# Performance work log

Hardware: AMD Instinct MI355X
Metric: run time of the kernel (lower is better)

The kernel has to match this reference:

```python
import jax, jax.numpy as jnp
import numpy as np

EPS = 1e-5
GROUPS = 8

def _bn(x, g, b, axes):
    # training-mode batch norm over `axes`, channel axis = 1
    m = jnp.mean(x, axis=axes, keepdims=True)
    v = jnp.var(x, axis=axes, keepdims=True)
    shp = (1, -1) + (1,) * (x.ndim - 2)
    return (x - m) / jnp.sqrt(v + EPS) * g.reshape(shp) + b.reshape(shp)

def setup_inputs() -> dict:
    key = jax.random.key(0)
    k0, k1, k2 = jax.random.split(key, 3)
    N, C, T, V = 64, 256, 64, 25
    out_planes = 256
    gp = out_planes // GROUPS  # 32
    x = jax.random.normal(k0, (N, C, T, V), jnp.float32)
    w_qkv = jax.random.normal(k1, (2 * out_planes, C), jnp.float32) * np.float32(np.sqrt(1.0 / C))
    relative = jax.random.normal(k2, (2 * gp, 2 * V - 1), jnp.float32) * np.float32(np.sqrt(1.0 / gp))
    return {
        "x": x,
        "w_qkv": w_qkv,
        "relative": relative,
        "bn_qkv_g": jnp.ones(2 * out_planes, jnp.float32),
        "bn_qkv_b": jnp.zeros(2 * out_planes, jnp.float32),
        "bn_sim_g": jnp.ones(3 * GROUPS, jnp.float32),
        "bn_sim_b": jnp.zeros(3 * GROUPS, jnp.float32),
        "bn_out_g": jnp.ones(2 * out_planes, jnp.float32),
        "bn_out_b": jnp.zeros(2 * out_planes, jnp.float32),
    }

def reference(x, w_qkv, relative, bn_qkv_g, bn_qkv_b, bn_sim_g, bn_sim_b, bn_out_g, bn_out_b):
    N, C, T, V = x.shape
    out_planes = w_qkv.shape[0] // 2
    gp = out_planes // GROUPS
    K = V  # kernel_size == V by construction
    # static relative index table
    qi = np.arange(K)[None, :]
    ki = np.arange(K)[:, None]
    flat_idx = (ki - qi + K - 1).reshape(-1)
    # mean over frames T (permute(0,2,1,3) then mean over dim1 == mean over axis 2)
    y = jnp.mean(x, axis=2)  # [N, C, V]
    # 1x1 conv qkv + BN1d
    qkv = _bn(jnp.einsum('oc,ncv->nov', w_qkv, y), bn_qkv_g, bn_qkv_b, (0, 2))
    qkv = qkv.reshape(N, GROUPS, 2 * gp, V)
    q, k, v = qkv[:, :, : gp // 2], qkv[:, :, gp // 2: gp], qkv[:, :, gp:]
    all_emb = relative[:, flat_idx].reshape(2 * gp, K, K)
    q_e, k_e, v_e = all_emb[: gp // 2], all_emb[gp // 2: gp], all_emb[gp:]
    qr = jnp.einsum('ngci,cij->ngij', q, q_e)
    kr = jnp.einsum('ngci,cij->ngij', k, k_e).swapaxes(2, 3)
    qk = jnp.einsum('ngci,ngcj->ngij', q, k)
    stacked = jnp.concatenate([qk, qr, kr], axis=1)  # [N, 3*groups, V, V]
    stacked = _bn(stacked, bn_sim_g, bn_sim_b, (0, 2, 3)).reshape(N, 3, GROUPS, V, V).sum(axis=1)
    sim = jax.nn.softmax(stacked, axis=3)  # [N, groups, V, V]
    sv = jnp.einsum('ngij,ngcj->ngci', sim, v)
    sve = jnp.einsum('ngij,cij->ngci', sim, v_e)
    so = jnp.concatenate([sv, sve], axis=-1).reshape(N, 2 * out_planes, V)
    o = _bn(so, bn_out_g, bn_out_b, (0, 2)).reshape(N, out_planes, 2, V).sum(axis=2)
    o = jax.nn.sigmoid(o)[:, :, None, :]  # [N, out_planes, 1, V]
    return x + x * o
```

## Files before the change

kernel.cpp:

```cpp
#include <hip/hip_runtime.h>
#include <cmath>

#define NN 64
#define CC 256
#define TT 64
#define VV 25
#define OO 512
#define GG 8
#define NV (NN*VV)
#define STK 625

typedef float f4 __attribute__((ext_vector_type(4)));

__global__ __launch_bounds__(256) void k_mean(const float* __restrict__ x,
                                              float* __restrict__ y,
                                              float* __restrict__ accz) {
    __shared__ float tile[TT * VV];
    __shared__ float part[8][VV];
    int b = blockIdx.x;
    if (b == 0) {
        for (int i = threadIdx.x; i < 2096; i += 256) accz[i] = 0.f;
    }
    const float4* x4 = (const float4*)(x + (size_t)b * (TT * VV));
    float4* t4 = (float4*)tile;
    for (int i = threadIdx.x; i < (TT * VV) / 4; i += 256) t4[i] = x4[i];
    __syncthreads();
    int t = threadIdx.x;
    if (t < 200) {
        int v = t % VV, ch = t / VV;
        float s = 0.f;
        #pragma unroll
        for (int k = 0; k < 8; ++k) s += tile[(ch * 8 + k) * VV + v];
        part[ch][v] = s;
    }
    __syncthreads();
    if (t < VV) {
        float s = 0.f;
        #pragma unroll
        for (int k = 0; k < 8; ++k) s += part[k][t];
        y[(size_t)b * VV + t] = s * (1.0f / TT);
    }
}

__global__ __launch_bounds__(256) void k_qkv(const float* __restrict__ y,
                                             const float* __restrict__ w,
                                             float* __restrict__ qkv,
                                             float* __restrict__ qacc) {
    __shared__ float ys[CC][VV + 1];
    __shared__ float qs[64][VV + 1];
    int n = blockIdx.x >> 3, oc = blockIdx.x & 7;
    const float* yp = y + (size_t)n * CC * VV;
    for (int i = threadIdx.x; i < CC * VV; i += 256) ys[i / VV][i % VV] = yp[i];
    __syncthreads();
    int t = threadIdx.x;
    if (t < 200) {
        int v = t % VV, o0 = t / VV;
        const float* wp = w + (size_t)(oc * 64 + o0) * CC;
        float acc[8] = {0, 0, 0, 0, 0, 0, 0, 0};
        for (int c = 0; c < CC; c += 8) {
            float y0 = ys[c][v],     y1 = ys[c + 1][v], y2 = ys[c + 2][v], y3 = ys[c + 3][v];
            float y4_ = ys[c + 4][v], y5 = ys[c + 5][v], y6 = ys[c + 6][v], y7 = ys[c + 7][v];
            #pragma unroll
            for (int u = 0; u < 8; ++u) {
                const float4 wa = *(const float4*)(wp + (size_t)u * 8 * CC + c);
                const float4 wb = *(const float4*)(wp + (size_t)u * 8 * CC + c + 4);
                acc[u] += y0 * wa.x + y1 * wa.y + y2 * wa.z + y3 * wa.w
                        + y4_ * wb.x + y5 * wb.y + y6 * wb.z + y7 * wb.w;
            }
        }
        #pragma unroll
        for (int u = 0; u < 8; ++u) qs[o0 + u * 8][v] = acc[u];
    }
    __syncthreads();
    float* qp = qkv + ((size_t)n * OO + oc * 64) * VV;
    for (int i = t; i < 64 * VV; i += 256) qp[i] = qs[i / VV][i % VV];
    if (t < 64) {
        float s = 0.f, s2 = 0.f;
        #pragma unroll
        for (int v = 0; v < VV; ++v) { float val = qs[t][v]; s += val; s2 += val * val; }
        atomicAdd(&qacc[oc * 64 + t], s);
        atomicAdd(&qacc[512 + oc * 64 + t], s2);
    }
}

__global__ __launch_bounds__(256) void k_scores(const float* __restrict__ qkv,
                                                const float* __restrict__ rel,
                                                const float* __restrict__ qacc,
                                                const float* __restrict__ gq,
                                                const float* __restrict__ bq,
                                                float* __restrict__ stk,
                                                float* __restrict__ sacc) {
    int n = blockIdx.x >> 3, gb = blockIdx.x & 7;
    __shared__ float qs[32][VV + 1];
    __shared__ float rs[32 * 49];
    __shared__ float csc[32], csh[32];
    __shared__ float sred[24];
    int t = threadIdx.x;
    if (t < 32) {
        int ch = gb * 64 + t;
        float m = qacc[ch] * (1.0f / NV);
        float var = qacc[512 + ch] * (1.0f / NV) - m * m;
        float sc = gq[ch] * rsqrtf(var + 1e-5f);
        csc[t] = sc; csh[t] = bq[ch] - m * sc;
    }
    __syncthreads();
    for (int i = t; i < 32 * VV; i += 256) {
        int c = i / VV, v = i - c * VV;
        qs[c][v] = qkv[((size_t)n * OO + gb * 64 + c) * VV + v] * csc[c] + csh[c];
    }
    for (int i = t; i < 32 * 49; i += 256) rs[i] = rel[i];
    __syncthreads();
    float ls0 = 0.f, ls1 = 0.f, ls2 = 0.f, ls3 = 0.f, ls4 = 0.f, ls5 = 0.f;
    size_t base = (size_t)n * 24;
    for (int ij = t; ij < STK; ij += 256) {
        int i = ij / VV, j = ij - (ij / VV) * VV;
        float aqk = 0.f, aqr = 0.f, akr = 0.f;
        #pragma unroll
        for (int c = 0; c < 16; ++c) {
            float qv = qs[c][i], kv = qs[16 + c][j];
            aqk += qv * kv;
            aqr += qv * rs[c * 49 + i - j + 24];
            akr += kv * rs[(16 + c) * 49 + j - i + 24];
        }
        stk[(base + gb) * STK + ij]      = aqk;
        stk[(base + 8 + gb) * STK + ij]  = aqr;
        stk[(base + 16 + gb) * STK + ij] = akr;
        ls0 += aqk; ls1 += aqk * aqk;
        ls2 += aqr; ls3 += aqr * aqr;
        ls4 += akr; ls5 += akr * akr;
    }
    #pragma unroll
    for (int off = 32; off > 0; off >>= 1) {
        ls0 += __shfl_down(ls0, off); ls1 += __shfl_down(ls1, off);
        ls2 += __shfl_down(ls2, off); ls3 += __shfl_down(ls3, off);
        ls4 += __shfl_down(ls4, off); ls5 += __shfl_down(ls5, off);
    }
    int lane = t & 63, wid = t >> 6;
    if (lane == 0) {
        sred[wid * 6 + 0] = ls0; sred[wid * 6 + 1] = ls1;
        sred[wid * 6 + 2] = ls2; sred[wid * 6 + 3] = ls3;
        sred[wid * 6 + 4] = ls4; sred[wid * 6 + 5] = ls5;
    }
    __syncthreads();
    if (t < 6) {
        float t2 = sred[t] + sred[6 + t] + sred[12 + t] + sred[18 + t];
        int ch = (t >> 1) * 8 + gb;
        atomicAdd(&sacc[(t & 1) * 24 + ch], t2);
    }
}

__global__ __launch_bounds__(256) void k_attnout(const float* __restrict__ stk,
                                                 const float* __restrict__ qkv,
                                                 const float* __restrict__ rel,
                                                 const float* __restrict__ qacc,
                                                 const float* __restrict__ gq,
                                                 const float* __restrict__ bq,
                                                 const float* __restrict__ sacc,
                                                 const float* __restrict__ gs,
                                                 const float* __restrict__ bs,
                                                 float* __restrict__ so,
                                                 float* __restrict__ oacc) {
    int n = blockIdx.x >> 3, gb = blockIdx.x & 7;
    __shared__ float S[STK];
    __shared__ float vs[32][VV + 1];
    __shared__ float rs[32 * 49];
    __shared__ float svs[800], sves[800];
    __shared__ float csc[32], csh[32];
    __shared__ float simp[6];
    int t = threadIdx.x;
    if (t < 32) {
        int ch = gb * 64 + 32 + t;
        float m = qacc[ch] * (1.0f / NV);
        float var = qacc[512 + ch] * (1.0f / NV) - m * m;
        float sc = gq[ch] * rsqrtf(var + 1e-5f);
        csc[t] = sc; csh[t] = bq[ch] - m * sc;
    }
    if (t < 3) {
        int ch = t * 8 + gb;
        float m = sacc[ch] * (1.0f / 40000.0f);
        float var = sacc[24 + ch] * (1.0f / 40000.0f) - m * m;
        float sc = gs[ch] * rsqrtf(var + 1e-5f);
        simp[t * 2] = sc; simp[t * 2 + 1] = bs[ch] - m * sc;
    }
    __syncthreads();
    const size_t sb = (size_t)n * 24 * STK;
    for (int ij = t; ij < STK; ij += 256)
        S[ij] = stk[sb + (size_t)gb * STK + ij] * simp[0] + simp[1]
              + stk[sb + (size_t)(8 + gb) * STK + ij] * simp[2] + simp[3]
              + stk[sb + (size_t)(16 + gb) * STK + ij] * simp[4] + simp[5];
    for (int i = t; i < 32 * VV; i += 256) {
        int c = i / VV, v = i - (i / VV) * VV;
        vs[c][v] = qkv[((size_t)n * OO + gb * 64 + 32 + c) * VV + v] * csc[c] + csh[c];
    }
    for (int i = t; i < 32 * 49; i += 256) rs[i] = rel[32 * 49 + i];
    __syncthreads();
    if (t < 200) {
        int i = t >> 3, l = t & 7;
        float mx = -1e30f;
        for (int j = l; j < VV; j += 8) mx = fmaxf(mx, S[i * VV + j]);
        #pragma unroll
        for (int off = 4; off > 0; off >>= 1) mx = fmaxf(mx, __shfl_xor(mx, off));
        float sum = 0.f;
        for (int j = l; j < VV; j += 8) {
            float e = expf(S[i * VV + j] - mx);
            S[i * VV + j] = e;
            sum += e;
        }
        #pragma unroll
        for (int off = 4; off > 0; off >>= 1) sum += __shfl_xor(sum, off);
        float inv = 1.0f / sum;
        for (int j = l; j < VV; j += 8) S[i * VV + j] *= inv;
    }
    __syncthreads();
    for (int idx = t; idx < 800; idx += 256) {
        int c = idx / VV, i = idx - (idx / VV) * VV;
        float sv = 0.f, sve = 0.f;
        #pragma unroll
        for (int j = 0; j < VV; ++j) {
            float p = S[i * VV + j];
            sv  += p * vs[c][j];
            sve += p * rs[c * 49 + i - j + 24];
        }
        svs[idx] = sv; sves[idx] = sve;
    }
    __syncthreads();
    if (t < 64) {
        int c = t >> 1;
        const float* src = (t & 1) ? (sves + c * VV) : (svs + c * VV);
        float s = 0.f, s2 = 0.f;
        #pragma unroll
        for (int i = 0; i < VV; ++i) { float val = src[i]; s += val; s2 += val * val; }
        atomicAdd(&oacc[gb * 64 + t], s);
        atomicAdd(&oacc[512 + gb * 64 + t], s2);
    }
    float* sop = so + ((size_t)n * OO + gb * 64) * VV;
    for (int idx = t; idx < 1600; idx += 256) {
        int oc = idx / VV, i = idx - (idx / VV) * VV;
        int c = oc >> 1;
        sop[idx] = (oc & 1) ? sves[c * VV + i] : svs[c * VV + i];
    }
}

__global__ __launch_bounds__(256) void k_final(const float* __restrict__ x,
                                               const float* __restrict__ so,
                                               const float* __restrict__ oacc,
                                               const float* __restrict__ go,
                                               const float* __restrict__ bo,
                                               float* __restrict__ out) {
    int b = (NN * CC - 1) - blockIdx.x;
    int n = b >> 8, p = b & 255;
    __shared__ float orow[VV];
    if (threadIdx.x < VV) {
        int o0 = 2 * p, o1 = 2 * p + 1;
        float m0 = oacc[o0] * (1.0f / NV);
        float var0 = oacc[512 + o0] * (1.0f / NV) - m0 * m0;
        float sc0 = go[o0] * rsqrtf(var0 + 1e-5f), sh0 = bo[o0] - m0 * sc0;
        float m1 = oacc[o1] * (1.0f / NV);
        float var1 = oacc[512 + o1] * (1.0f / NV) - m1 * m1;
        float sc1 = go[o1] * rsqrtf(var1 + 1e-5f), sh1 = bo[o1] - m1 * sc1;
        int v = threadIdx.x;
        float a  = so[((size_t)n * OO + o0) * VV + v] * sc0 + sh0;
        float c2 = so[((size_t)n * OO + o1) * VV + v] * sc1 + sh1;
        float z = a + c2;
        orow[v] = 1.0f + 1.0f / (1.0f + expf(-z));
    }
    __syncthreads();
    const f4* x4 = (const f4*)(x + (size_t)b * (TT * VV));
    f4* y4 = (f4*)(out + (size_t)b * (TT * VV));
    for (int wv = threadIdx.x; wv < (TT * VV) / 4; wv += 256) {
        f4 xv = __builtin_nontemporal_load(&x4[wv]);
        int e = 4 * wv;
        int v0 = e % VV;
        f4 r;
        int v;
        v = v0;                      r.x = xv.x * orow[v];
        v = v0 + 1; if (v >= VV) v -= VV; r.y = xv.y * orow[v];
        v = v0 + 2; if (v >= VV) v -= VV; r.z = xv.z * orow[v];
        v = v0 + 3; if (v >= VV) v -= VV; r.w = xv.w * orow[v];
        __builtin_nontemporal_store(r, &y4[wv]);
    }
}

extern "C" void kernel_launch(void* const* d_in, const int* in_sizes, int n_in,
                              void* d_out, int out_size, void* d_ws, size_t ws_size,
                              hipStream_t stream) {
    (void)in_sizes; (void)n_in; (void)out_size; (void)ws_size;
    const float* x        = (const float*)d_in[0];
    const float* w_qkv    = (const float*)d_in[1];
    const float* relative = (const float*)d_in[2];
    const float* bn_qkv_g = (const float*)d_in[3];
    const float* bn_qkv_b = (const float*)d_in[4];
    const float* bn_sim_g = (const float*)d_in[5];
    const float* bn_sim_b = (const float*)d_in[6];
    const float* bn_out_g = (const float*)d_in[7];
    const float* bn_out_b = (const float*)d_in[8];
    float* out = (float*)d_out;

    float* ws = (float*)d_ws;
    float* w_y    = ws;
    float* w_qkvp = ws + 409600;
    float* w_stk  = ws + 1228800;
    float* w_so   = ws + 2188800;
    float* qacc   = ws + 3008000;
    float* sacc   = qacc + 1024;
    float* oacc   = sacc + 48;

    k_mean<<<NN * CC, 256, 0, stream>>>(x, w_y, qacc);
    k_qkv<<<NN * 8, 256, 0, stream>>>(w_y, w_qkv, w_qkvp, qacc);
    k_scores<<<NN * GG, 256, 0, stream>>>(w_qkvp, relative, qacc, bn_qkv_g, bn_qkv_b, w_stk, sacc);
    k_attnout<<<NN * GG, 256, 0, stream>>>(w_stk, w_qkvp, relative, qacc, bn_qkv_g, bn_qkv_b,
                                           sacc, bn_sim_g, bn_sim_b, w_so, oacc);
    k_final<<<NN * CC, 256, 0, stream>>>(x, w_so, oacc, bn_out_g, bn_out_b, out);
}
```

Measured before the change: 277.0 us.

## Recompute attention scores in attnout instead of storing stacked scores buffer

The scores kernel now only accumulates batch-norm statistics, split four ways per (n, group) with separate atomic banks, and no longer writes the stacked score tensor to global memory. The attention-output kernel recomputes qk, qr and kr from the normalized qkv and relative embeddings, then applies the BN scale directly. The per-channel BN shift is dropped because softmax is invariant to adding a constant along a row. This removes a global write/read round trip of roughly 1M floats at the cost of doing the score arithmetic twice and using more shared memory in attnout.

Result: no change. 281.2 us (+1.5%).

```diff
diff --git a/kernel.cpp b/kernel.cpp
--- a/kernel.cpp
+++ b/kernel.cpp
@@ -19,7 +19,7 @@
     __shared__ float part[8][VV];
     int b = blockIdx.x;
     if (b == 0) {
-        for (int i = threadIdx.x; i < 2096; i += 256) accz[i] = 0.f;
+        for (int i = threadIdx.x; i < 2240; i += 256) accz[i] = 0.f;
     }
     const float4* x4 = (const float4*)(x + (size_t)b * (TT * VV));
     float4* t4 = (float4*)tile;
@@ -83,14 +83,14 @@
     }
 }
 
-__global__ __launch_bounds__(256) void k_scores(const float* __restrict__ qkv,
+__global__ __launch_bounds__(256) void k_sstats(const float* __restrict__ qkv,
                                                 const float* __restrict__ rel,
                                                 const float* __restrict__ qacc,
                                                 const float* __restrict__ gq,
                                                 const float* __restrict__ bq,
-                                                float* __restrict__ stk,
                                                 float* __restrict__ sacc) {
-    int n = blockIdx.x >> 3, gb = blockIdx.x & 7;
+    int blk = blockIdx.x;
+    int n = blk >> 5, r = blk & 31, gb = r >> 2, split = r & 3;
     __shared__ float qs[32][VV + 1];
     __shared__ float rs[32 * 49];
     __shared__ float csc[32], csh[32];
@@ -111,23 +111,22 @@
     for (int i = t; i < 32 * 49; i += 256) rs[i] = rel[i];
     __syncthreads();
     float ls0 = 0.f, ls1 = 0.f, ls2 = 0.f, ls3 = 0.f, ls4 = 0.f, ls5 = 0.f;
-    size_t base = (size_t)n * 24;
-    for (int ij = t; ij < STK; ij += 256) {
-        int i = ij / VV, j = ij - (ij / VV) * VV;
-        float aqk = 0.f, aqr = 0.f, akr = 0.f;
-        #pragma unroll
-        for (int c = 0; c < 16; ++c) {
-            float qv = qs[c][i], kv = qs[16 + c][j];
-            aqk += qv * kv;
-            aqr += qv * rs[c * 49 + i - j + 24];
-            akr += kv * rs[(16 + c) * 49 + j - i + 24];
-        }
-        stk[(base + gb) * STK + ij]      = aqk;
-        stk[(base + 8 + gb) * STK + ij]  = aqr;
-        stk[(base + 16 + gb) * STK + ij] = akr;
-        ls0 += aqk; ls1 += aqk * aqk;
-        ls2 += aqr; ls3 += aqr * aqr;
-        ls4 += akr; ls5 += akr * akr;
+    for (int idx = t; idx < 157; idx += 256) {
+        int ij = split + 4 * idx;
+        if (ij < STK) {
+            int i = ij / VV, j = ij - (ij / VV) * VV;
+            float aqk = 0.f, aqr = 0.f, akr = 0.f;
+            #pragma unroll
+            for (int c = 0; c < 16; ++c) {
+                float qv = qs[c][i], kv = qs[16 + c][j];
+                aqk += qv * kv;
+                aqr += qv * rs[c * 49 + i - j + 24];
+                akr += kv * rs[(16 + c) * 49 + j - i + 24];
+            }
+            ls0 += aqk; ls1 += aqk * aqk;
+            ls2 += aqr; ls3 += aqr * aqr;
+            ls4 += akr; ls5 += akr * akr;
+        }
     }
     #pragma unroll
     for (int off = 32; off > 0; off >>= 1) {
@@ -145,54 +144,67 @@
     if (t < 6) {
         float t2 = sred[t] + sred[6 + t] + sred[12 + t] + sred[18 + t];
         int ch = (t >> 1) * 8 + gb;
-        atomicAdd(&sacc[(t & 1) * 24 + ch], t2);
-    }
-}
-
-__global__ __launch_bounds__(256) void k_attnout(const float* __restrict__ stk,
-                                                 const float* __restrict__ qkv,
+        atomicAdd(&sacc[split * 48 + (t & 1) * 24 + ch], t2);
+    }
+}
+
+__global__ __launch_bounds__(256) void k_attnout(const float* __restrict__ qkv,
                                                  const float* __restrict__ rel,
                                                  const float* __restrict__ qacc,
                                                  const float* __restrict__ gq,
                                                  const float* __restrict__ bq,
                                                  const float* __restrict__ sacc,
                                                  const float* __restrict__ gs,
-                                                 const float* __restrict__ bs,
                                                  float* __restrict__ so,
                                                  float* __restrict__ oacc) {
     int n = blockIdx.x >> 3, gb = blockIdx.x & 7;
     __shared__ float S[STK];
-    __shared__ float vs[32][VV + 1];
-    __shared__ float rs[32 * 49];
+    __shared__ float qk_s[64][VV + 1];
+    __shared__ float rs[64 * 49];
     __shared__ float svs[800], sves[800];
-    __shared__ float csc[32], csh[32];
-    __shared__ float simp[6];
+    __shared__ float csc[64], csh[64];
+    __shared__ float simp[3];
     int t = threadIdx.x;
-    if (t < 32) {
-        int ch = gb * 64 + 32 + t;
+    if (t < 64) {
+        int ch = gb * 64 + t;
         float m = qacc[ch] * (1.0f / NV);
         float var = qacc[512 + ch] * (1.0f / NV) - m * m;
         float sc = gq[ch] * rsqrtf(var + 1e-5f);
         csc[t] = sc; csh[t] = bq[ch] - m * sc;
     }
-    if (t < 3) {
-        int ch = t * 8 + gb;
-        float m = sacc[ch] * (1.0f / 40000.0f);
-        float var = sacc[24 + ch] * (1.0f / 40000.0f) - m * m;
-        float sc = gs[ch] * rsqrtf(var + 1e-5f);
-        simp[t * 2] = sc; simp[t * 2 + 1] = bs[ch] - m * sc;
-    }
-    __syncthreads();
-    const size_t sb = (size_t)n * 24 * STK;
-    for (int ij = t; ij < STK; ij += 256)
-        S[ij] = stk[sb + (size_t)gb * STK + ij] * simp[0] + simp[1]
-              + stk[sb + (size_t)(8 + gb) * STK + ij] * simp[2] + simp[3]
-              + stk[sb + (size_t)(16 + gb) * STK + ij] * simp[4] + simp[5];
-    for (int i = t; i < 32 * VV; i += 256) {
+    if (t >= 64 && t < 67) {
+        int k = t - 64;
+        int ch = k * 8 + gb;
+        float s = 0.f, s2 = 0.f;
+        #pragma unroll
+        for (int bnk = 0; bnk < 4; ++bnk) {
+            s  += sacc[bnk * 48 + ch];
+            s2 += sacc[bnk * 48 + 24 + ch];
+        }
+        float m = s * (1.0f / 40000.0f);
+        float var = s2 * (1.0f / 40000.0f) - m * m;
+        simp[k] = gs[ch] * rsqrtf(var + 1e-5f);
+    }
+    __syncthreads();
+    for (int i = t; i < 64 * VV; i += 256) {
         int c = i / VV, v = i - (i / VV) * VV;
-        vs[c][v] = qkv[((size_t)n * OO + gb * 64 + 32 + c) * VV + v] * csc[c] + csh[c];
-    }
-    for (int i = t; i < 32 * 49; i += 256) rs[i] = rel[32 * 49 + i];
+        qk_s[c][v] = qkv[((size_t)n * OO + gb * 64 + c) * VV + v] * csc[c] + csh[c];
+    }
+    for (int i = t; i < 64 * 49; i += 256) rs[i] = rel[i];
+    __syncthreads();
+    float s0 = simp[0], s1 = simp[1], s2 = simp[2];
+    for (int ij = t; ij < STK; ij += 256) {
+        int i = ij / VV, j = ij - (ij / VV) * VV;
+        float aqk = 0.f, aqr = 0.f, akr = 0.f;
+        #pragma unroll
+        for (int c = 0; c < 16; ++c) {
+            float qv = qk_s[c][i], kv = qk_s[16 + c][j];
+            aqk += qv * kv;
+            aqr += qv * rs[c * 49 + i - j + 24];
+            akr += kv * rs[(16 + c) * 49 + j - i + 24];
+        }
+        S[ij] = aqk * s0 + aqr * s1 + akr * s2;
+    }
     __syncthreads();
     if (t < 200) {
         int i = t >> 3, l = t & 7;
@@ -218,8 +230,8 @@
         #pragma unroll
         for (int j = 0; j < VV; ++j) {
             float p = S[i * VV + j];
-            sv  += p * vs[c][j];
-            sve += p * rs[c * 49 + i - j + 24];
+            sv  += p * qk_s[32 + c][j];
+            sve += p * rs[(32 + c) * 49 + i - j + 24];
         }
         svs[idx] = sv; sves[idx] = sve;
     }
@@ -227,11 +239,11 @@
     if (t < 64) {
         int c = t >> 1;
         const float* src = (t & 1) ? (sves + c * VV) : (svs + c * VV);
-        float s = 0.f, s2 = 0.f;
-        #pragma unroll
-        for (int i = 0; i < VV; ++i) { float val = src[i]; s += val; s2 += val * val; }
+        float s = 0.f, sq = 0.f;
+        #pragma unroll
+        for (int i = 0; i < VV; ++i) { float val = src[i]; s += val; sq += val * val; }
         atomicAdd(&oacc[gb * 64 + t], s);
-        atomicAdd(&oacc[512 + gb * 64 + t], s2);
+        atomicAdd(&oacc[512 + gb * 64 + t], sq);
     }
     float* sop = so + ((size_t)n * OO + gb * 64) * VV;
     for (int idx = t; idx < 1600; idx += 256) {
@@ -294,21 +306,21 @@
     const float* bn_sim_b = (const float*)d_in[6];
     const float* bn_out_g = (const float*)d_in[7];
     const float* bn_out_b = (const float*)d_in[8];
+    (void)bn_sim_b;
     float* out = (float*)d_out;
 
     float* ws = (float*)d_ws;
     float* w_y    = ws;
     float* w_qkvp = ws + 409600;
-    float* w_stk  = ws + 1228800;
-    float* w_so   = ws + 2188800;
-    float* qacc   = ws + 3008000;
+    float* w_so   = ws + 1228800;
+    float* qacc   = ws + 2048000;
     float* sacc   = qacc + 1024;
-    float* oacc   = sacc + 48;
+    float* oacc   = sacc + 192;
 
     k_mean<<<NN * CC, 256, 0, stream>>>(x, w_y, qacc);
     k_qkv<<<NN * 8, 256, 0, stream>>>(w_y, w_qkv, w_qkvp, qacc);
-    k_scores<<<NN * GG, 256, 0, stream>>>(w_qkvp, relative, qacc, bn_qkv_g, bn_qkv_b, w_stk, sacc);
-    k_attnout<<<NN * GG, 256, 0, stream>>>(w_stk, w_qkvp, relative, qacc, bn_qkv_g, bn_qkv_b,
-                                           sacc, bn_sim_g, bn_sim_b, w_so, oacc);
+    k_sstats<<<NN * GG * 4, 256, 0, stream>>>(w_qkvp, relative, qacc, bn_qkv_g, bn_qkv_b, sacc);
+    k_attnout<<<NN * GG, 256, 0, stream>>>(w_qkvp, relative, qacc, bn_qkv_g, bn_qkv_b,
+                                           sacc, bn_sim_g, w_so, oacc);
     k_final<<<NN * CC, 256, 0, stream>>>(x, w_so, oacc, bn_out_g, bn_out_b, out);
 }
```
